# Kernel tuning notes

Hardware: AMD Instinct MI355X
Metric: run time of the kernel (lower is better)

Reference implementation:

```python
import math
import jax, jax.numpy as jnp
import numpy as np

DIM = 256; DEPTH = 5; FANOUT = 10; VOCAB = 257
B = 16; T = 2048
NEXP = 8; HID = 512; TOPK = 2; TEMP = 1.0; HEADS = 2
CAPACITY = math.ceil(B * TOPK / NEXP * 1.1)  # capacity-based dispatch, =5
LAYER_SIZES = [FANOUT ** l for l in range(DEPTH)]  # [1,10,100,1000,10000]


def setup_inputs() -> dict:
    key = jax.random.key(0)
    ks = iter(jax.random.split(key, 64))
    def p(shape, scale=0.02):
        return jax.random.normal(next(ks), shape, jnp.float32) * scale
    inp = {
        'tokens': jax.random.randint(next(ks), (B, T), 0, VOCAB),
        'embed': p((VOCAB, DIM)),
        'pin_w': p((DIM, DIM)), 'pin_b': jnp.zeros(DIM, jnp.float32),
        'pch_w': p((DIM, DIM)), 'pch_b': jnp.zeros(DIM, jnp.float32),
        'depth_bias': p((DEPTH, DIM)),
        'q_w': p((DIM, DIM)), 'q_b': jnp.zeros(DIM, jnp.float32),
        'k_w': p((DIM, DIM)), 'k_b': jnp.zeros(DIM, jnp.float32),
        'v_w': p((DIM, DIM)), 'v_b': jnp.zeros(DIM, jnp.float32),
        'o_w': p((DIM, DIM)), 'o_b': jnp.zeros(DIM, jnp.float32),
        'level_gate': jnp.zeros(DEPTH, jnp.float32),
        'depth_gate': jnp.zeros((DEPTH, DIM), jnp.float32),
        'in_proj_w': p((DIM, 3 * DIM)), 'in_proj_b': jnp.zeros(3 * DIM, jnp.float32),
        'out_proj_w': p((DIM, DIM)), 'out_proj_b': jnp.zeros(DIM, jnp.float32),
        'ln_g': jnp.ones(DIM, jnp.float32), 'ln_b': jnp.zeros(DIM, jnp.float32),
        'ic_gate': jnp.zeros(1, jnp.float32),
        'gate_w': p((DIM, NEXP)), 'gate_b': jnp.zeros(NEXP, jnp.float32),
        'ew1': p((NEXP, DIM, HID)), 'eb1': jnp.zeros((NEXP, HID), jnp.float32),
        'ew2': p((NEXP, HID, DIM)), 'eb2': jnp.zeros((NEXP, DIM), jnp.float32),
        'hw1': p((DIM, DIM)), 'hb1': jnp.zeros(DIM, jnp.float32),
        'hw2': p((DIM, VOCAB)), 'hb2': jnp.zeros(VOCAB, jnp.float32),
    }
    return inp


def _fractal(context, pin_w, pin_b, pch_w, pch_b, depth_bias, q_w, q_b, k_w, k_b,
             v_w, v_b, o_w, o_b, level_gate, depth_gate,
             in_proj_w, in_proj_b, out_proj_w, out_proj_b, ln_g, ln_b, ic_gate):
    Bc = context.shape[0]
    base = context @ pin_w + pin_b                       # [B,D]
    y_next = None
    level_means = [None] * DEPTH
    inv_sqrt_d = 1.0 / math.sqrt(DIM)
    for l in reversed(range(DEPTH)):
        n = LAYER_SIZES[l]
        if l == DEPTH - 1:
            child_agg = jnp.zeros((Bc, n, DIM), context.dtype)
        else:
            yg = y_next.reshape(Bc, n, FANOUT, DIM)      # children grouped per parent
            q = (base + depth_bias[l]) @ q_w + q_b       # [B,D], shared across nodes
            k = yg @ k_w + k_b
            v = yg @ v_w + v_b
            att = jax.nn.softmax(jnp.einsum('bd,bnfd->bnf', q, k) * inv_sqrt_d, axis=-1)
            child_agg = jax.nn.sigmoid(depth_gate[l]) * jnp.einsum('bnf,bnfd->bnd', att, v)
        gate = jax.nn.sigmoid(level_gate[l])
        upd = (base[:, None, :] + depth_bias[l][None, None, :] + child_agg @ pch_w + pch_b) * gate
        y = jax.nn.relu(upd) @ o_w + o_b                 # [B,n,D]
        level_means[l] = y.mean(axis=1)
        y_next = y
    root = y_next[:, 0, :]                               # n==1 at level 0
    # interconnect: MHA over per-level means [B,DEPTH,D]
    z = jnp.stack(level_means, axis=1)
    qkv = z @ in_proj_w + in_proj_b
    qh, kh, vh = jnp.split(qkv, 3, axis=-1)
    hd = DIM // HEADS
    def to_heads(t):
        return t.reshape(Bc, DEPTH, HEADS, hd).transpose(0, 2, 1, 3)
    qh, kh, vh = to_heads(qh), to_heads(kh), to_heads(vh)
    aw = jax.nn.softmax(jnp.einsum('bhqd,bhkd->bhqk', qh, kh) / math.sqrt(hd), axis=-1)
    z2 = jnp.einsum('bhqk,bhkd->bhqd', aw, vh).transpose(0, 2, 1, 3).reshape(Bc, DEPTH, DIM)
    z2 = z2 @ out_proj_w + out_proj_b
    zs = z + z2
    mu = zs.mean(-1, keepdims=True)
    var = ((zs - mu) ** 2).mean(-1, keepdims=True)
    zn = (zs - mu) / jnp.sqrt(var + 1e-5) * ln_g + ln_b
    return root + jax.nn.sigmoid(ic_gate) * zn[:, 0, :]


def _moe(ctx, gate_w, gate_b, ew1, eb1, ew2, eb2):
    scaled = (ctx @ gate_w + gate_b) / TEMP
    top_vals, top_idx = jax.lax.top_k(scaled, TOPK)      # [B,K]
    gs = jax.nn.softmax(top_vals, axis=-1)               # [B,K], strictly > 0
    out = jnp.zeros_like(ctx)
    for e in range(NEXP):                                # fixed small expert loop
        sflat = jnp.where(top_idx == e, gs, -1.0).reshape(-1)   # [B*K]
        vals, pos = jax.lax.top_k(sflat, CAPACITY)       # capacity-limited dispatch
        w = jnp.where(vals > 0.0, vals, 0.0)             # drop unassigned/overflow
        tok = pos // TOPK
        xin = ctx[tok]                                   # [cap,D]
        eo = jax.nn.relu(xin @ ew1[e] + eb1[e]) @ ew2[e] + eb2[e]
        out = out.at[tok].add(eo * w[:, None])
    return out


def reference(tokens, embed, pin_w, pin_b, pch_w, pch_b, depth_bias,
              q_w, q_b, k_w, k_b, v_w, v_b, o_w, o_b, level_gate, depth_gate,
              in_proj_w, in_proj_b, out_proj_w, out_proj_b, ln_g, ln_b, ic_gate,
              gate_w, gate_b, ew1, eb1, ew2, eb2, hw1, hb1, hw2, hb2):
    x = embed[tokens]                                    # [B,T,D]
    context = x.mean(axis=1)                             # [B,D]
    root = _fractal(context, pin_w, pin_b, pch_w, pch_b, depth_bias, q_w, q_b,
                    k_w, k_b, v_w, v_b, o_w, o_b, level_gate, depth_gate,
                    in_proj_w, in_proj_b, out_proj_w, out_proj_b, ln_g, ln_b, ic_gate)
    root = root + _moe(root, gate_w, gate_b, ew1, eb1, ew2, eb2)
    h = x + root[:, None, :]                             # per-token logits from context + token emb
    logits = jax.nn.relu(h @ hw1 + hb1) @ hw2 + hb2      # [B,T,V]
    return logits
```

## Files before the change

### kernel.cpp

```cpp
#include <hip/hip_runtime.h>
#include <hip/hip_bf16.h>
#include <math.h>

#define DIM    256
#define DEPTH  5
#define FANOUT 10
#define VOCAB  257
#define BB     16
#define TT     2048
#define NEXP   8
#define HID    512
#define TOPK   2
#define CAP    5
#define TSTR   260

__device__ __forceinline__ float sigm(float x) { return 1.f / (1.f + expf(-x)); }

__device__ __forceinline__ float dotcol64(const float* sv, const float* __restrict__ W,
                                          int col, int k0, int stride) {
  float acc = 0.f;
#pragma unroll 8
  for (int i = 0; i < 64; ++i) {
    int k = k0 + i;
    acc = fmaf(sv[k], W[(size_t)k * stride + col], acc);
  }
  return acc;
}

__global__ void __launch_bounds__(1024) k_fractal(
    const int* __restrict__ tokens, const float* __restrict__ embed,
    const float* __restrict__ pin_w, const float* __restrict__ pin_b,
    const float* __restrict__ pch_w, const float* __restrict__ pch_b,
    const float* __restrict__ depth_bias,
    const float* __restrict__ v_w, const float* __restrict__ v_b,
    const float* __restrict__ o_w, const float* __restrict__ o_b,
    const float* __restrict__ level_gate, const float* __restrict__ depth_gate,
    const float* __restrict__ in_proj_w, const float* __restrict__ in_proj_b,
    const float* __restrict__ out_proj_w, const float* __restrict__ out_proj_b,
    const float* __restrict__ ln_g, const float* __restrict__ ln_b,
    const float* __restrict__ ic_gate,
    float* __restrict__ rootA) {
  int b = blockIdx.x;
  int tid = threadIdx.x;
  int d = tid & 255;
  int ks = tid >> 8;
  int k0 = ks * 64;
  __shared__ int cnt[VOCAB];
  __shared__ float sv[DIM];
  __shared__ float basev[DIM];
  __shared__ float ym[DEPTH][DIM];
  __shared__ float q0v[DIM], kh[DEPTH][DIM], vh[DEPTH][DIM];
  __shared__ float red4[4][DIM];
  __shared__ float red11[4][11][DIM];
  __shared__ float zsv[DIM];
  __shared__ float aw[16];
  __shared__ float redl[8];

  for (int i = tid; i < VOCAB; i += 1024) cnt[i] = 0;
  __syncthreads();
  for (int t = tid; t < TT; t += 1024) atomicAdd(&cnt[tokens[b * TT + t]], 1);
  __syncthreads();
  {
    float acc = 0.f;
#pragma unroll
    for (int h = 0; h < 2; ++h) {
      int vb = ks * 64 + h * 32;
      float ev[32], cv[32];
#pragma unroll
      for (int i = 0; i < 32; ++i) ev[i] = embed[(size_t)(vb + i) * DIM + d];
#pragma unroll
      for (int i = 0; i < 32; ++i) cv[i] = (float)cnt[vb + i];
#pragma unroll
      for (int i = 0; i < 32; ++i) acc = fmaf(cv[i], ev[i], acc);
    }
    if (ks == 0) acc = fmaf((float)cnt[256], embed[(size_t)256 * DIM + d], acc);
    red4[ks][d] = acc;
  }
  __syncthreads();
  if (ks == 0)
    sv[d] = (red4[0][d] + red4[1][d] + red4[2][d] + red4[3][d]) * (1.0f / (float)TT);
  __syncthreads();

  red4[ks][d] = dotcol64(sv, pin_w, d, k0, DIM);
  __syncthreads();
  if (ks == 0) {
    float base = red4[0][d] + red4[1][d] + red4[2][d] + red4[3][d] + pin_b[d];
    basev[d] = base;
    float u = (base + depth_bias[4 * DIM + d] + pch_b[d]) * sigm(level_gate[4]);
    sv[d] = fmaxf(u, 0.f);
  }
  __syncthreads();
  red4[ks][d] = dotcol64(sv, o_w, d, k0, DIM);
  __syncthreads();
  if (ks == 0) {
    float y = red4[0][d] + red4[1][d] + red4[2][d] + red4[3][d] + o_b[d];
    ym[4][d] = y;
    sv[d] = y;
  }
  __syncthreads();
  for (int l = 3; l >= 0; --l) {
    red4[ks][d] = dotcol64(sv, v_w, d, k0, DIM);
    __syncthreads();
    if (ks == 0) {
      float vv = red4[0][d] + red4[1][d] + red4[2][d] + red4[3][d] + v_b[d];
      sv[d] = sigm(depth_gate[l * DIM + d]) * vv;
    }
    __syncthreads();
    red4[ks][d] = dotcol64(sv, pch_w, d, k0, DIM);
    __syncthreads();
    if (ks == 0) {
      float t = red4[0][d] + red4[1][d] + red4[2][d] + red4[3][d] + pch_b[d];
      float u = (basev[d] + depth_bias[l * DIM + d] + t) * sigm(level_gate[l]);
      sv[d] = fmaxf(u, 0.f);
    }
    __syncthreads();
    red4[ks][d] = dotcol64(sv, o_w, d, k0, DIM);
    __syncthreads();
    if (ks == 0) {
      float y = red4[0][d] + red4[1][d] + red4[2][d] + red4[3][d] + o_b[d];
      ym[l][d] = y;
      sv[d] = y;
    }
    __syncthreads();
  }
  {
    float aq = 0.f;
    float ak0 = 0.f, ak1 = 0.f, ak2 = 0.f, ak3 = 0.f, ak4 = 0.f;
    float av0 = 0.f, av1 = 0.f, av2 = 0.f, av3 = 0.f, av4 = 0.f;
#pragma unroll
    for (int h = 0; h < 8; ++h) {
      int kb = k0 + h * 8;
      float wq[8], wk[8], wv8[8];
#pragma unroll
      for (int i = 0; i < 8; ++i) {
        const float* wrow = in_proj_w + (size_t)(kb + i) * 768;
        wq[i] = wrow[d]; wk[i] = wrow[256 + d]; wv8[i] = wrow[512 + d];
      }
#pragma unroll
      for (int i = 0; i < 8; ++i) {
        float z0 = ym[0][kb + i];
        aq  = fmaf(z0, wq[i], aq);
        ak0 = fmaf(z0, wk[i], ak0);
        av0 = fmaf(z0, wv8[i], av0);
        float z1 = ym[1][kb + i];
        ak1 = fmaf(z1, wk[i], ak1);
        av1 = fmaf(z1, wv8[i], av1);
        float z2 = ym[2][kb + i];
        ak2 = fmaf(z2, wk[i], ak2);
        av2 = fmaf(z2, wv8[i], av2);
        float z3 = ym[3][kb + i];
        ak3 = fmaf(z3, wk[i], ak3);
        av3 = fmaf(z3, wv8[i], av3);
        float z4 = ym[4][kb + i];
        ak4 = fmaf(z4, wk[i], ak4);
        av4 = fmaf(z4, wv8[i], av4);
      }
    }
    red11[ks][0][d] = ak0; red11[ks][1][d] = ak1; red11[ks][2][d] = ak2;
    red11[ks][3][d] = ak3; red11[ks][4][d] = ak4;
    red11[ks][5][d] = av0; red11[ks][6][d] = av1; red11[ks][7][d] = av2;
    red11[ks][8][d] = av3; red11[ks][9][d] = av4;
    red11[ks][10][d] = aq;
  }
  __syncthreads();
  for (int idx = tid; idx < 11 * DIM; idx += 1024) {
    int c = idx >> 8, dd = idx & 255;
    float sum = red11[0][c][dd] + red11[1][c][dd] + red11[2][c][dd] + red11[3][c][dd];
    if (c < 5)       kh[c][dd]     = sum + in_proj_b[256 + dd];
    else if (c < 10) vh[c - 5][dd] = sum + in_proj_b[512 + dd];
    else             q0v[dd]       = sum + in_proj_b[dd];
  }
  __syncthreads();
  if (tid < 10) {
    int h = tid / 5, l = tid - h * 5;
    float s = 0.f;
    for (int j = 0; j < 128; ++j) s = fmaf(q0v[h * 128 + j], kh[l][h * 128 + j], s);
    aw[tid] = s * 0.08838834764831845f;
  }
  __syncthreads();
  if (tid < 2) {
    float m = aw[tid * 5];
    for (int l = 1; l < 5; ++l) m = fmaxf(m, aw[tid * 5 + l]);
    float e[5], ssum = 0.f;
    for (int l = 0; l < 5; ++l) { e[l] = expf(aw[tid * 5 + l] - m); ssum += e[l]; }
    for (int l = 0; l < 5; ++l) aw[tid * 5 + l] = e[l] / ssum;
  }
  __syncthreads();
  if (ks == 0) {
    int h = d >> 7;
    float z2 = 0.f;
    for (int l = 0; l < 5; ++l) z2 = fmaf(aw[h * 5 + l], vh[l][d], z2);
    sv[d] = z2;
  }
  __syncthreads();
  red4[ks][d] = dotcol64(sv, out_proj_w, d, k0, DIM);
  __syncthreads();
  if (ks == 0) {
    float z2p = red4[0][d] + red4[1][d] + red4[2][d] + red4[3][d] + out_proj_b[d];
    zsv[d] = ym[0][d] + z2p;
  }
  __syncthreads();
  float zs = 0.f, df = 0.f, mu = 0.f;
  if (tid < 256) {
    zs = zsv[tid];
    float v = zs;
    for (int o = 32; o > 0; o >>= 1) v += __shfl_down(v, o, 64);
    if ((tid & 63) == 0) redl[tid >> 6] = v;
  }
  __syncthreads();
  if (tid < 256) {
    mu = (redl[0] + redl[1] + redl[2] + redl[3]) * (1.f / 256.f);
    df = zs - mu;
  }
  __syncthreads();
  if (tid < 256) {
    float v = df * df;
    for (int o = 32; o > 0; o >>= 1) v += __shfl_down(v, o, 64);
    if ((tid & 63) == 0) redl[tid >> 6] = v;
  }
  __syncthreads();
  if (tid < 256) {
    float var = (redl[0] + redl[1] + redl[2] + redl[3]) * (1.f / 256.f);
    float zn = df / sqrtf(var + 1e-5f) * ln_g[tid] + ln_b[tid];
    rootA[b * DIM + tid] = ym[0][tid] + sigm(ic_gate[0]) * zn;
  }
}

__global__ void __launch_bounds__(1024) k_gate(const float* __restrict__ rootA,
                                               const float* __restrict__ gate_w,
                                               const float* __restrict__ gate_b,
                                               int* __restrict__ etok,
                                               float* __restrict__ ewt,
                                               float* __restrict__ root2) {
  __shared__ float red[BB * NEXP][9];
  __shared__ float sc[BB * NEXP];
  __shared__ float gs[BB * TOPK];
  __shared__ int gidx[BB * TOPK];
  int tid = threadIdx.x;
  int be = tid >> 3, ks = tid & 7;
  int b = be >> 3, e = be & 7;
  {
    float acc = 0.f;
#pragma unroll 8
    for (int i = 0; i < 32; ++i) {
      int k = ks * 32 + i;
      acc = fmaf(rootA[b * DIM + k], gate_w[k * NEXP + e], acc);
    }
    red[be][ks] = acc;
  }
  for (int i = tid; i < BB * DIM; i += 1024) root2[i] = rootA[i];
  __syncthreads();
  if (tid < BB * NEXP) {
    float s = gate_b[tid & 7];
#pragma unroll
    for (int g = 0; g < 8; ++g) s += red[tid][g];
    sc[tid] = s;
  }
  __syncthreads();
  if (tid < BB) {
    int bb = tid;
    int i0 = 0; float v0 = sc[bb * 8 + 0];
    for (int ee = 1; ee < 8; ++ee) { float v = sc[bb * 8 + ee]; if (v > v0) { v0 = v; i0 = ee; } }
    int i1 = -1; float v1 = -1e30f;
    for (int ee = 0; ee < 8; ++ee) {
      if (ee == i0) continue;
      float v = sc[bb * 8 + ee];
      if (v > v1) { v1 = v; i1 = ee; }
    }
    float e1 = expf(v1 - v0);
    float s = 1.f + e1;
    gs[bb * 2 + 0] = 1.f / s;  gidx[bb * 2 + 0] = i0;
    gs[bb * 2 + 1] = e1 / s;   gidx[bb * 2 + 1] = i1;
  }
  __syncthreads();
  if (tid < NEXP) {
    int ee = tid;
    float vals[32];
    bool used[32];
    for (int i = 0; i < 32; ++i) { vals[i] = (gidx[i] == ee) ? gs[i] : -1.0f; used[i] = false; }
    for (int s = 0; s < CAP; ++s) {
      int bi = -1; float bv = -1e30f;
      for (int i = 0; i < 32; ++i) {
        if (used[i]) continue;
        if (vals[i] > bv) { bv = vals[i]; bi = i; }
      }
      used[bi] = true;
      etok[ee * CAP + s] = bi >> 1;
      ewt[ee * CAP + s] = bv > 0.f ? bv : 0.f;
    }
  }
}

__global__ void __launch_bounds__(256) k_expert1(
    const float* __restrict__ rootA,
    const float* __restrict__ ew1, const float* __restrict__ eb1,
    const int* __restrict__ etok,
    float* __restrict__ hid_ws) {
  int bx = blockIdx.x;
  int e = bx >> 3, jt = bx & 7, j0 = jt * 64;
  int tid = threadIdx.x, w = tid >> 6, lane = tid & 63;
  __shared__ float xin[CAP][DIM];
  __shared__ float red[CAP][4][64];
  __shared__ int stok[CAP];
  if (tid < CAP) stok[tid] = etok[e * CAP + tid];
  __syncthreads();
  for (int idx = tid; idx < CAP * DIM; idx += 256) {
    int s = idx >> 8, k = idx & 255;
    xin[s][k] = rootA[stok[s] * DIM + k];
  }
  __syncthreads();
  float a0 = 0.f, a1 = 0.f, a2 = 0.f, a3 = 0.f, a4 = 0.f;
  const float* W = ew1 + (size_t)e * DIM * HID + j0 + lane;
  int kbase = w * 64;
#pragma unroll
  for (int h = 0; h < 8; ++h) {
    float wv[8];
#pragma unroll
    for (int i = 0; i < 8; ++i) wv[i] = W[(size_t)(kbase + h * 8 + i) * HID];
#pragma unroll
    for (int i = 0; i < 8; ++i) {
      int k = kbase + h * 8 + i;
      a0 = fmaf(xin[0][k], wv[i], a0);
      a1 = fmaf(xin[1][k], wv[i], a1);
      a2 = fmaf(xin[2][k], wv[i], a2);
      a3 = fmaf(xin[3][k], wv[i], a3);
      a4 = fmaf(xin[4][k], wv[i], a4);
    }
  }
  red[0][w][lane] = a0; red[1][w][lane] = a1; red[2][w][lane] = a2;
  red[3][w][lane] = a3; red[4][w][lane] = a4;
  __syncthreads();
  for (int idx = tid; idx < CAP * 64; idx += 256) {
    int s = idx >> 6, j = idx & 63;
    float sum = red[s][0][j] + red[s][1][j] + red[s][2][j] + red[s][3][j]
              + eb1[e * HID + j0 + j];
    hid_ws[((size_t)(e * CAP + s)) * HID + j0 + j] = fmaxf(sum, 0.f);
  }
}

__global__ void __launch_bounds__(256) k_expert2(
    const float* __restrict__ hid_ws,
    const float* __restrict__ ew2, const float* __restrict__ eb2,
    const float* __restrict__ ewt, const int* __restrict__ etok,
    float* __restrict__ root2) {
  int bx = blockIdx.x;
  int e = bx >> 3, dt = bx & 7, d0 = dt * 32;
  int tid = threadIdx.x, seg = tid >> 5, c = tid & 31;
  __shared__ float hv[CAP][HID];
  __shared__ float red[CAP][8][32];
  for (int idx = tid; idx < CAP * HID; idx += 256) {
    int s = idx >> 9, k = idx & 511;
    hv[s][k] = hid_ws[((size_t)(e * CAP + s)) * HID + k];
  }
  __syncthreads();
  float a0 = 0.f, a1 = 0.f, a2 = 0.f, a3 = 0.f, a4 = 0.f;
  const float* W = ew2 + (size_t)e * HID * DIM + d0 + c;
  int kbase = seg * 64;
#pragma unroll
  for (int h = 0; h < 8; ++h) {
    float wv[8];
#pragma unroll
    for (int i = 0; i < 8; ++i) wv[i] = W[(size_t)(kbase + h * 8 + i) * DIM];
#pragma unroll
    for (int i = 0; i < 8; ++i) {
      int k = kbase + h * 8 + i;
      a0 = fmaf(hv[0][k], wv[i], a0);
      a1 = fmaf(hv[1][k], wv[i], a1);
      a2 = fmaf(hv[2][k], wv[i], a2);
      a3 = fmaf(hv[3][k], wv[i], a3);
      a4 = fmaf(hv[4][k], wv[i], a4);
    }
  }
  red[0][seg][c] = a0; red[1][seg][c] = a1; red[2][seg][c] = a2;
  red[3][seg][c] = a3; red[4][seg][c] = a4;
  __syncthreads();
  if (tid < CAP * 32) {
    int s = tid >> 5, cc = tid & 31;
    float sum = 0.f;
#pragma unroll
    for (int g = 0; g < 8; ++g) sum += red[s][g][cc];
    sum += eb2[e * DIM + d0 + cc];
    float w = ewt[e * CAP + s];
    if (w > 0.f)
      atomicAdd(&root2[etok[e * CAP + s] * DIM + d0 + cc], sum * w);
  }
}

__global__ void __launch_bounds__(256) k_table(
    const float* __restrict__ embed, const float* __restrict__ root2,
    const float* __restrict__ hw1, const float* __restrict__ hb1,
    const float* __restrict__ hw2, const float* __restrict__ hb2,
    float* __restrict__ table) {
  int tok = blockIdx.x, r0 = blockIdx.y * 4;
  int c = threadIdx.x;
  __shared__ float hrow[4][DIM];
  __shared__ float hid[4][DIM];
  __shared__ float tailred[4][17];
  {
    float ev = embed[(size_t)tok * DIM + c];
#pragma unroll
    for (int j = 0; j < 4; ++j) hrow[j][c] = ev + root2[(size_t)(r0 + j) * DIM + c];
  }
  __syncthreads();
  {
    float a0 = hb1[c], a1 = a0, a2 = a0, a3 = a0;
    for (int kb = 0; kb < DIM; kb += 8) {
      float wv[8];
#pragma unroll
      for (int i = 0; i < 8; ++i) wv[i] = hw1[(size_t)(kb + i) * DIM + c];
#pragma unroll
      for (int i = 0; i < 8; ++i) {
        int k = kb + i;
        a0 = fmaf(hrow[0][k], wv[i], a0);
        a1 = fmaf(hrow[1][k], wv[i], a1);
        a2 = fmaf(hrow[2][k], wv[i], a2);
        a3 = fmaf(hrow[3][k], wv[i], a3);
      }
    }
    hid[0][c] = fmaxf(a0, 0.f); hid[1][c] = fmaxf(a1, 0.f);
    hid[2][c] = fmaxf(a2, 0.f); hid[3][c] = fmaxf(a3, 0.f);
  }
  __syncthreads();
  {
    float a0 = hb2[c], a1 = a0, a2 = a0, a3 = a0;
    for (int kb = 0; kb < DIM; kb += 8) {
      float wv[8];
#pragma unroll
      for (int i = 0; i < 8; ++i) wv[i] = hw2[(size_t)(kb + i) * VOCAB + c];
#pragma unroll
      for (int i = 0; i < 8; ++i) {
        int k = kb + i;
        a0 = fmaf(hid[0][k], wv[i], a0);
        a1 = fmaf(hid[1][k], wv[i], a1);
        a2 = fmaf(hid[2][k], wv[i], a2);
        a3 = fmaf(hid[3][k], wv[i], a3);
      }
    }
    table[((size_t)((r0 + 0) * VOCAB + tok)) * TSTR + c] = a0;
    table[((size_t)((r0 + 1) * VOCAB + tok)) * TSTR + c] = a1;
    table[((size_t)((r0 + 2) * VOCAB + tok)) * TSTR + c] = a2;
    table[((size_t)((r0 + 3) * VOCAB + tok)) * TSTR + c] = a3;
  }
  if (c < 64) {
    int r = c >> 4, seg = c & 15;
    float sum = 0.f;
#pragma unroll 4
    for (int i = 0; i < 16; ++i) {
      int k = seg * 16 + i;
      sum = fmaf(hid[r][k], hw2[(size_t)k * VOCAB + 256], sum);
    }
    tailred[r][seg] = sum;
  }
  __syncthreads();
  if (c < 4) {
    float a = hb2[256];
#pragma unroll
    for (int s = 0; s < 16; ++s) a += tailred[c][s];
    table[((size_t)((r0 + c) * VOCAB + tok)) * TSTR + 256] = a;
  }
}

__global__ void __launch_bounds__(1024) k_scatter(const int* __restrict__ tokens,
                                                  const float* __restrict__ table,
                                                  float* __restrict__ out) {
  int f = blockIdx.x * 1024 + threadIdx.x;
  int row = (int)((unsigned)f / 257u);
  int c = f - row * 257;
  int b = row >> 11;
  int tok = tokens[row];
  out[f] = table[((size_t)(b * VOCAB + tok)) * TSTR + c];
}

extern "C" void kernel_launch(void* const* d_in, const int* in_sizes, int n_in,
                              void* d_out, int out_size, void* d_ws, size_t ws_size,
                              hipStream_t stream) {
  (void)in_sizes; (void)n_in; (void)out_size; (void)ws_size;
  const int*   tokens     = (const int*)d_in[0];
  const float* embed      = (const float*)d_in[1];
  const float* pin_w      = (const float*)d_in[2];
  const float* pin_b      = (const float*)d_in[3];
  const float* pch_w      = (const float*)d_in[4];
  const float* pch_b      = (const float*)d_in[5];
  const float* depth_bias = (const float*)d_in[6];
  const float* v_w        = (const float*)d_in[11];
  const float* v_b        = (const float*)d_in[12];
  const float* o_w        = (const float*)d_in[13];
  const float* o_b        = (const float*)d_in[14];
  const float* level_gate = (const float*)d_in[15];
  const float* depth_gate = (const float*)d_in[16];
  const float* in_proj_w  = (const float*)d_in[17];
  const float* in_proj_b  = (const float*)d_in[18];
  const float* out_proj_w = (const float*)d_in[19];
  const float* out_proj_b = (const float*)d_in[20];
  const float* ln_g       = (const float*)d_in[21];
  const float* ln_b       = (const float*)d_in[22];
  const float* ic_gate    = (const float*)d_in[23];
  const float* gate_w     = (const float*)d_in[24];
  const float* gate_b     = (const float*)d_in[25];
  const float* ew1        = (const float*)d_in[26];
  const float* eb1        = (const float*)d_in[27];
  const float* ew2        = (const float*)d_in[28];
  const float* eb2        = (const float*)d_in[29];
  const float* hw1        = (const float*)d_in[30];
  const float* hb1        = (const float*)d_in[31];
  const float* hw2        = (const float*)d_in[32];
  const float* hb2        = (const float*)d_in[33];
  float* out = (float*)d_out;

  float* ws      = (float*)d_ws;
  float* rootA   = ws + 4096;
  float* root2   = ws + 8192;
  int*   etok    = (int*)(ws + 22528);
  float* ewt     = ws + 22576;
  float* table   = ws + 22656;
  float* hid_ws  = table;

  k_fractal<<<BB, 1024, 0, stream>>>(tokens, embed, pin_w, pin_b, pch_w, pch_b,
                                     depth_bias, v_w, v_b, o_w, o_b, level_gate,
                                     depth_gate, in_proj_w, in_proj_b, out_proj_w,
                                     out_proj_b, ln_g, ln_b, ic_gate, rootA);
  k_gate<<<1, 1024, 0, stream>>>(rootA, gate_w, gate_b, etok, ewt, root2);
  k_expert1<<<NEXP * 8, 256, 0, stream>>>(rootA, ew1, eb1, etok, hid_ws);
  k_expert2<<<NEXP * 8, 256, 0, stream>>>(hid_ws, ew2, eb2, ewt, etok, root2);
  k_table<<<dim3(VOCAB, 4), 256, 0, stream>>>(embed, root2, hw1, hb1, hw2, hb2, table);
  k_scatter<<<(BB * TT * VOCAB) / 1024, 1024, 0, stream>>>(tokens, table, out);
}
```

Before: 268.9 us.

## Vectorize scatter stores, split fractal matvecs eight ways, widen table unroll

The output scatter now has each thread write a float4 of four consecutive logits, with a slow path for groups that cross a row boundary. This cuts the thread count by four and uses wide stores on the dominant memory-bound kernel. The fractal matvecs now split K into 8 slices, with each thread computing two output columns, so all 1024 threads do work. The k_table weight loads are unrolled by 16 instead of 8. The risk is that the unaligned gather reads from the padded table break up coalescing on the load side.

```diff
diff --git a/kernel.cpp b/kernel.cpp
--- a/kernel.cpp
+++ b/kernel.cpp
@@ -16,15 +16,18 @@
 
 __device__ __forceinline__ float sigm(float x) { return 1.f / (1.f + expf(-x)); }
 
-__device__ __forceinline__ float dotcol64(const float* sv, const float* __restrict__ W,
-                                          int col, int k0, int stride) {
-  float acc = 0.f;
+__device__ __forceinline__ void dotcol2(const float* sv, const float* __restrict__ W,
+                                        int p, int k0, float* r0, float* r1) {
+  float a0 = 0.f, a1 = 0.f;
 #pragma unroll 8
-  for (int i = 0; i < 64; ++i) {
+  for (int i = 0; i < 32; ++i) {
     int k = k0 + i;
-    acc = fmaf(sv[k], W[(size_t)k * stride + col], acc);
-  }
-  return acc;
+    float s = sv[k];
+    const float* row = W + (size_t)k * DIM;
+    a0 = fmaf(s, row[p], a0);
+    a1 = fmaf(s, row[p + 128], a1);
+  }
+  *r0 = a0; *r1 = a1;
 }
 
 __global__ void __launch_bounds__(1024) k_fractal(
@@ -45,12 +48,15 @@
   int d = tid & 255;
   int ks = tid >> 8;
   int k0 = ks * 64;
+  int p = tid & 127;
+  int ks8 = tid >> 7;
+  int k08 = ks8 * 32;
   __shared__ int cnt[VOCAB];
   __shared__ float sv[DIM];
   __shared__ float basev[DIM];
   __shared__ float ym[DEPTH][DIM];
   __shared__ float q0v[DIM], kh[DEPTH][DIM], vh[DEPTH][DIM];
-  __shared__ float red4[4][DIM];
+  __shared__ float redA[8][DIM];
   __shared__ float red11[4][11][DIM];
   __shared__ float zsv[DIM];
   __shared__ float aw[16];
@@ -74,52 +80,65 @@
       for (int i = 0; i < 32; ++i) acc = fmaf(cv[i], ev[i], acc);
     }
     if (ks == 0) acc = fmaf((float)cnt[256], embed[(size_t)256 * DIM + d], acc);
-    red4[ks][d] = acc;
-  }
-  __syncthreads();
-  if (ks == 0)
-    sv[d] = (red4[0][d] + red4[1][d] + red4[2][d] + red4[3][d]) * (1.0f / (float)TT);
-  __syncthreads();
-
-  red4[ks][d] = dotcol64(sv, pin_w, d, k0, DIM);
-  __syncthreads();
-  if (ks == 0) {
-    float base = red4[0][d] + red4[1][d] + red4[2][d] + red4[3][d] + pin_b[d];
-    basev[d] = base;
-    float u = (base + depth_bias[4 * DIM + d] + pch_b[d]) * sigm(level_gate[4]);
-    sv[d] = fmaxf(u, 0.f);
-  }
-  __syncthreads();
-  red4[ks][d] = dotcol64(sv, o_w, d, k0, DIM);
-  __syncthreads();
-  if (ks == 0) {
-    float y = red4[0][d] + red4[1][d] + red4[2][d] + red4[3][d] + o_b[d];
-    ym[4][d] = y;
-    sv[d] = y;
+    redA[ks][d] = acc;
+  }
+  __syncthreads();
+  if (tid < 256)
+    sv[tid] = (redA[0][tid] + redA[1][tid] + redA[2][tid] + redA[3][tid]) * (1.0f / (float)TT);
+  __syncthreads();
+
+  dotcol2(sv, pin_w, p, k08, &redA[ks8][p], &redA[ks8][p + 128]);
+  __syncthreads();
+  if (tid < 256) {
+    float s = 0.f;
+#pragma unroll
+    for (int g = 0; g < 8; ++g) s += redA[g][tid];
+    float base = s + pin_b[tid];
+    basev[tid] = base;
+    float u = (base + depth_bias[4 * DIM + tid] + pch_b[tid]) * sigm(level_gate[4]);
+    sv[tid] = fmaxf(u, 0.f);
+  }
+  __syncthreads();
+  dotcol2(sv, o_w, p, k08, &redA[ks8][p], &redA[ks8][p + 128]);
+  __syncthreads();
+  if (tid < 256) {
+    float s = 0.f;
+#pragma unroll
+    for (int g = 0; g < 8; ++g) s += redA[g][tid];
+    float y = s + o_b[tid];
+    ym[4][tid] = y; sv[tid] = y;
   }
   __syncthreads();
   for (int l = 3; l >= 0; --l) {
-    red4[ks][d] = dotcol64(sv, v_w, d, k0, DIM);
+    dotcol2(sv, v_w, p, k08, &redA[ks8][p], &redA[ks8][p + 128]);
     __syncthreads();
-    if (ks == 0) {
-      float vv = red4[0][d] + red4[1][d] + red4[2][d] + red4[3][d] + v_b[d];
-      sv[d] = sigm(depth_gate[l * DIM + d]) * vv;
+    if (tid < 256) {
+      float s = 0.f;
+#pragma unroll
+      for (int g = 0; g < 8; ++g) s += redA[g][tid];
+      float vv = s + v_b[tid];
+      sv[tid] = sigm(depth_gate[l * DIM + tid]) * vv;
     }
     __syncthreads();
-    red4[ks][d] = dotcol64(sv, pch_w, d, k0, DIM);
+    dotcol2(sv, pch_w, p, k08, &redA[ks8][p], &redA[ks8][p + 128]);
     __syncthreads();
-    if (ks == 0) {
-      float t = red4[0][d] + red4[1][d] + red4[2][d] + red4[3][d] + pch_b[d];
-      float u = (basev[d] + depth_bias[l * DIM + d] + t) * sigm(level_gate[l]);
-      sv[d] = fmaxf(u, 0.f);
+    if (tid < 256) {
+      float s = 0.f;
+#pragma unroll
+      for (int g = 0; g < 8; ++g) s += redA[g][tid];
+      float t = s + pch_b[tid];
+      float u = (basev[tid] + depth_bias[l * DIM + tid] + t) * sigm(level_gate[l]);
+      sv[tid] = fmaxf(u, 0.f);
     }
     __syncthreads();
-    red4[ks][d] = dotcol64(sv, o_w, d, k0, DIM);
+    dotcol2(sv, o_w, p, k08, &redA[ks8][p], &redA[ks8][p + 128]);
     __syncthreads();
-    if (ks == 0) {
-      float y = red4[0][d] + red4[1][d] + red4[2][d] + red4[3][d] + o_b[d];
-      ym[l][d] = y;
-      sv[d] = y;
+    if (tid < 256) {
+      float s = 0.f;
+#pragma unroll
+      for (int g = 0; g < 8; ++g) s += redA[g][tid];
+      float y = s + o_b[tid];
+      ym[l][tid] = y; sv[tid] = y;
     }
     __syncthreads();
   }
@@ -186,18 +205,21 @@
     for (int l = 0; l < 5; ++l) aw[tid * 5 + l] = e[l] / ssum;
   }
   __syncthreads();
-  if (ks == 0) {
-    int h = d >> 7;
+  if (tid < 256) {
+    int h = tid >> 7;
     float z2 = 0.f;
-    for (int l = 0; l < 5; ++l) z2 = fmaf(aw[h * 5 + l], vh[l][d], z2);
-    sv[d] = z2;
-  }
-  __syncthreads();
-  red4[ks][d] = dotcol64(sv, out_proj_w, d, k0, DIM);
-  __syncthreads();
-  if (ks == 0) {
-    float z2p = red4[0][d] + red4[1][d] + red4[2][d] + red4[3][d] + out_proj_b[d];
-    zsv[d] = ym[0][d] + z2p;
+    for (int l = 0; l < 5; ++l) z2 = fmaf(aw[h * 5 + l], vh[l][tid], z2);
+    sv[tid] = z2;
+  }
+  __syncthreads();
+  dotcol2(sv, out_proj_w, p, k08, &redA[ks8][p], &redA[ks8][p + 128]);
+  __syncthreads();
+  if (tid < 256) {
+    float s = 0.f;
+#pragma unroll
+    for (int g = 0; g < 8; ++g) s += redA[g][tid];
+    float z2p = s + out_proj_b[tid];
+    zsv[tid] = ym[0][tid] + z2p;
   }
   __syncthreads();
   float zs = 0.f, df = 0.f, mu = 0.f;
@@ -404,12 +426,12 @@
   __syncthreads();
   {
     float a0 = hb1[c], a1 = a0, a2 = a0, a3 = a0;
-    for (int kb = 0; kb < DIM; kb += 8) {
-      float wv[8];
-#pragma unroll
-      for (int i = 0; i < 8; ++i) wv[i] = hw1[(size_t)(kb + i) * DIM + c];
-#pragma unroll
-      for (int i = 0; i < 8; ++i) {
+    for (int kb = 0; kb < DIM; kb += 16) {
+      float wv[16];
+#pragma unroll
+      for (int i = 0; i < 16; ++i) wv[i] = hw1[(size_t)(kb + i) * DIM + c];
+#pragma unroll
+      for (int i = 0; i < 16; ++i) {
         int k = kb + i;
         a0 = fmaf(hrow[0][k], wv[i], a0);
         a1 = fmaf(hrow[1][k], wv[i], a1);
@@ -423,12 +445,12 @@
   __syncthreads();
   {
     float a0 = hb2[c], a1 = a0, a2 = a0, a3 = a0;
-    for (int kb = 0; kb < DIM; kb += 8) {
-      float wv[8];
-#pragma unroll
-      for (int i = 0; i < 8; ++i) wv[i] = hw2[(size_t)(kb + i) * VOCAB + c];
-#pragma unroll
-      for (int i = 0; i < 8; ++i) {
+    for (int kb = 0; kb < DIM; kb += 16) {
+      float wv[16];
+#pragma unroll
+      for (int i = 0; i < 16; ++i) wv[i] = hw2[(size_t)(kb + i) * VOCAB + c];
+#pragma unroll
+      for (int i = 0; i < 16; ++i) {
         int k = kb + i;
         a0 = fmaf(hid[0][k], wv[i], a0);
         a1 = fmaf(hid[1][k], wv[i], a1);
@@ -460,15 +482,33 @@
   }
 }
 
-__global__ void __launch_bounds__(1024) k_scatter(const int* __restrict__ tokens,
-                                                  const float* __restrict__ table,
-                                                  float* __restrict__ out) {
-  int f = blockIdx.x * 1024 + threadIdx.x;
+__global__ void __launch_bounds__(256) k_scatter(const int* __restrict__ tokens,
+                                                 const float* __restrict__ table,
+                                                 float* __restrict__ out) {
+  int q = blockIdx.x * 256 + threadIdx.x;
+  int f = q << 2;
   int row = (int)((unsigned)f / 257u);
-  int c = f - row * 257;
+  int c0 = f - row * 257;
   int b = row >> 11;
   int tok = tokens[row];
-  out[f] = table[((size_t)(b * VOCAB + tok)) * TSTR + c];
+  const float* src = table + ((size_t)(b * VOCAB + tok)) * TSTR;
+  float4 v;
+  if (c0 <= 253) {
+    v.x = src[c0]; v.y = src[c0 + 1]; v.z = src[c0 + 2]; v.w = src[c0 + 3];
+  } else {
+    int row1 = min(row + 1, BB * TT - 1);
+    int b1 = row1 >> 11;
+    int tok1 = tokens[row1];
+    const float* src1 = table + ((size_t)(b1 * VOCAB + tok1)) * TSTR;
+    float t[4];
+#pragma unroll
+    for (int j = 0; j < 4; ++j) {
+      int cc = c0 + j;
+      t[j] = (cc <= 256) ? src[cc] : src1[cc - 257];
+    }
+    v = make_float4(t[0], t[1], t[2], t[3]);
+  }
+  *(float4*)(out + f) = v;
 }
 
 extern "C" void kernel_launch(void* const* d_in, const int* in_sizes, int n_in,
@@ -523,5 +563,5 @@
   k_expert1<<<NEXP * 8, 256, 0, stream>>>(rootA, ew1, eb1, etok, hid_ws);
   k_expert2<<<NEXP * 8, 256, 0, stream>>>(hid_ws, ew2, eb2, ewt, etok, root2);
   k_table<<<dim3(VOCAB, 4), 256, 0, stream>>>(embed, root2, hw1, hb1, hw2, hb2, table);
-  k_scatter<<<(BB * TT * VOCAB) / 1024, 1024, 0, stream>>>(tokens, table, out);
-}
+  k_scatter<<<(BB * TT * VOCAB) / 1024, 256, 0, stream>>>(tokens, table, out);
+}
```

Result: slower. 279.0 us (+3.7%).
